# Kernel tuning notes

Hardware: AMD Instinct MI355X
Metric: run time of the kernel (lower is better)

## Reference

```python
import jax, jax.numpy as jnp
import numpy as np

V, E, HD, B, T, K = 50000, 256, 512, 64, 512, 16
H = HD // 2            # per-direction LSTM hidden size
START_IDX, STOP_IDX = K - 2, K - 1
NEG = -10000.0


def setup_inputs() -> dict:
    key = jax.random.key(0)
    ks = jax.random.split(key, 12)
    s = 0.05
    sentence = jax.random.randint(ks[0], (B, T), 0, V)
    emb = jax.random.normal(ks[1], (V, E), jnp.float32)
    w_ih_f = jax.random.normal(ks[2], (4 * H, E), jnp.float32) * s
    w_hh_f = jax.random.normal(ks[3], (4 * H, H), jnp.float32) * s
    b_f = jax.random.normal(ks[4], (4 * H,), jnp.float32) * s
    w_ih_b = jax.random.normal(ks[5], (4 * H, E), jnp.float32) * s
    w_hh_b = jax.random.normal(ks[6], (4 * H, H), jnp.float32) * s
    b_b = jax.random.normal(ks[7], (4 * H,), jnp.float32) * s
    w_out = jax.random.normal(ks[8], (K, HD), jnp.float32) * s
    b_out = jax.random.normal(ks[9], (K,), jnp.float32) * s
    transitions = jax.random.normal(ks[10], (K, K), jnp.float32)
    transitions = transitions.at[START_IDX, :].set(NEG)  # nothing transitions into START
    transitions = transitions.at[:, STOP_IDX].set(NEG)   # nothing transitions out of STOP
    return dict(sentence=sentence, emb=emb, w_ih_f=w_ih_f, w_hh_f=w_hh_f, b_f=b_f,
                w_ih_b=w_ih_b, w_hh_b=w_hh_b, b_b=b_b, w_out=w_out, b_out=b_out,
                transitions=transitions)


def _lstm(xs, w_ih, w_hh, b):
    # xs: [T, B, E] -> hs: [T, B, H]; PyTorch gate order i,f,g,o; bias b = b_ih + b_hh
    Bn = xs.shape[1]
    def step(carry, x):
        h, c = carry
        g = x @ w_ih.T + h @ w_hh.T + b
        i, f, gg, o = jnp.split(g, 4, axis=-1)
        c = jax.nn.sigmoid(f) * c + jax.nn.sigmoid(i) * jnp.tanh(gg)
        h = jax.nn.sigmoid(o) * jnp.tanh(c)
        return (h, c), h
    init = (jnp.zeros((Bn, H), xs.dtype), jnp.zeros((Bn, H), xs.dtype))
    return jax.lax.scan(step, init, xs)[1]


def _lstm_feats(sentence, emb, w_ih_f, w_hh_f, b_f, w_ih_b, w_hh_b, b_b, w_out, b_out):
    x = emb[sentence].transpose(1, 0, 2)                 # [T, B, E]
    hf = _lstm(x, w_ih_f, w_hh_f, b_f)                   # forward direction
    hb = _lstm(x[::-1], w_ih_b, w_hh_b, b_b)[::-1]       # backward direction
    h = jnp.concatenate([hf, hb], axis=-1)               # [T, B, HD]
    return h @ w_out.T + b_out                           # [T, B, K]


def _viterbi(feats, transitions):
    # feats: [T, B, K]
    Bn = feats.shape[1]
    init = jnp.full((Bn, K), NEG, jnp.float32).at[:, START_IDX].set(0.0)
    def vstep(fv, feat):
        scores = fv[:, None, :] + transitions[None, :, :]  # [B, next, prev]
        return jnp.max(scores, axis=2) + feat, jnp.argmax(scores, axis=2)
    fv, bptrs = jax.lax.scan(vstep, init, feats)           # bptrs: [T, B, K]
    terminal = fv + transitions[STOP_IDX][None, :]
    best_score = jnp.max(terminal, axis=1)                 # [B]
    best_tag = jnp.argmax(terminal, axis=1)                # [B]
    def bstep(tag, bptr):
        prev = jnp.take_along_axis(bptr, tag[:, None], axis=1)[:, 0]
        return prev, tag
    _, path = jax.lax.scan(bstep, best_tag, bptrs, reverse=True)  # [T, B]
    return best_score, path


def reference(sentence, emb, w_ih_f, w_hh_f, b_f, w_ih_b, w_hh_b, b_b, w_out, b_out, transitions):
    feats = _lstm_feats(sentence, emb, w_ih_f, w_hh_f, b_f, w_ih_b, w_hh_b, b_b, w_out, b_out)
    score, tag_seq = _viterbi(feats, transitions)
    return score, tag_seq
```

## Files before the change

kernel.cpp:

```cpp
#include <hip/hip_runtime.h>
#include <math.h>

typedef _Float16 h2_t  __attribute__((ext_vector_type(2)));
typedef _Float16 h8_t  __attribute__((ext_vector_type(8)));
typedef _Float16 h16_t __attribute__((ext_vector_type(16)));
typedef _Float16 h32_t __attribute__((ext_vector_type(32)));
typedef float    f4_t  __attribute__((ext_vector_type(4)));

#define T_ 512
#define B_ 64
#define E_ 256
#define H_ 256
#define G_ 1024
#define K_ 16
#define NEG_ (-10000.0f)
#define START_ 14
#define STOP_ 15

#if defined(__has_builtin)
#if __has_builtin(__builtin_amdgcn_fdot2)
#define HAVE_FDOT2 1
#endif
#endif

static __device__ __forceinline__ float dot2(h2_t a, h2_t b, float c) {
#ifdef HAVE_FDOT2
    return __builtin_amdgcn_fdot2(a, b, c, false);
#else
    return fmaf((float)a[0], (float)b[0], fmaf((float)a[1], (float)b[1], c));
#endif
}

template <int P, typename V>
static __device__ __forceinline__ h2_t get2(V v) {
    return __builtin_shufflevector(v, v, 2 * P, 2 * P + 1);
}

__global__ __launch_bounds__(256)
void prep_weights(const float* __restrict__ w_hh_f,
                  const float* __restrict__ w_hh_b,
                  const float* __restrict__ w_ih_f,
                  const float* __restrict__ w_ih_b,
                  _Float16* __restrict__ wreg,
                  _Float16* __restrict__ wlds,
                  _Float16* __restrict__ wih16)
{
    const int blk = blockIdx.x, tid = threadIdx.x;
    if (blk < 48) {
        int idx = blk * 256 + tid;
        int dir = idx / 6144, rem = idx % 6144;
        int v = rem / 512, q = rem % 512;
        int row = (v < 6) ? q : q + 512;
        int kb = (v % 6) * 32;
        const float* src = (dir ? w_hh_b : w_hh_f) + (size_t)row * 256 + kb;
        _Float16* dst = wreg + (size_t)idx * 32;
        #pragma unroll
        for (int i = 0; i < 32; ++i) dst[i] = (_Float16)src[i];
    } else if (blk < 112) {
        int idx = (blk - 48) * 256 + tid;
        int dir = idx / 8192, rem = idx % 8192;
        int j = rem / 512, q = rem % 512;
        int p = j / 8, c = j % 8;
        int row = (c < 4) ? q : q + 512;
        int kb = 192 + (c & 3) * 16 + p * 8;
        const float* src = (dir ? w_hh_b : w_hh_f) + (size_t)row * 256 + kb;
        _Float16* dst = wlds + (size_t)idx * 8;
        #pragma unroll
        for (int i = 0; i < 8; ++i) dst[i] = (_Float16)src[i];
    } else {
        int idx = (blk - 112) * 256 + tid;
        int dir = idx / 32768, rem = idx % 32768;
        const float* src = (dir ? w_ih_b : w_ih_f) + (size_t)rem * 8;
        _Float16* dst = wih16 + (size_t)idx * 8;
        #pragma unroll
        for (int i = 0; i < 8; ++i) dst[i] = (_Float16)src[i];
    }
}

__global__ __launch_bounds__(256)
void gates_mfma(const int* __restrict__ sentence,
                const float* __restrict__ emb,
                const _Float16* __restrict__ wih16,
                _Float16* __restrict__ gin_f,
                _Float16* __restrict__ gin_b)
{
    __shared__ _Float16 As[64 * 264];
    __shared__ _Float16 Bs[256 * 40];
    __shared__ int sidx[64];

    const int bm  = blockIdx.x;
    const int dir = blockIdx.y;
    const int tid = threadIdx.x;

    const _Float16* __restrict__ wih = wih16 + (size_t)dir * 262144;
    _Float16* __restrict__ gout      = dir ? gin_b : gin_f;

    if (tid < 64) sidx[tid] = sentence[tid * T_ + bm];
    __syncthreads();

    {
        const int r = tid & 63, kq = tid >> 6;
        const float4* src = (const float4*)(emb + (size_t)sidx[r] * 256 + kq * 64);
        _Float16* dst = As + r * 264 + kq * 64;
        #pragma unroll
        for (int c = 0; c < 8; ++c) {
            float4 v0 = src[2 * c], v1 = src[2 * c + 1];
            h8_t o;
            o[0] = (_Float16)v0.x; o[1] = (_Float16)v0.y;
            o[2] = (_Float16)v0.z; o[3] = (_Float16)v0.w;
            o[4] = (_Float16)v1.x; o[5] = (_Float16)v1.y;
            o[6] = (_Float16)v1.z; o[7] = (_Float16)v1.w;
            *(h8_t*)(dst + c * 8) = o;
        }
    }

    const int wave = tid >> 6, lane = tid & 63;
    const int l15 = lane & 15, quad = lane >> 4;

    for (int pass = 0; pass < 4; ++pass) {
        const int n0 = pass * 256;
        f4_t acc[16];
        #pragma unroll
        for (int nt = 0; nt < 16; ++nt) acc[nt] = (f4_t){0.f, 0.f, 0.f, 0.f};

        for (int kc = 0; kc < 8; ++kc) {
            __syncthreads();
            {
                const h8_t* bsrc = (const h8_t*)(wih + (size_t)(n0 + tid) * 256 + kc * 32);
                #pragma unroll
                for (int c = 0; c < 4; ++c)
                    *(h8_t*)(Bs + tid * 40 + c * 8) = bsrc[c];
            }
            __syncthreads();
            h8_t a = *(const h8_t*)(As + (wave * 16 + l15) * 264 + kc * 32 + quad * 8);
            #pragma unroll
            for (int nt = 0; nt < 16; ++nt) {
                h8_t b = *(const h8_t*)(Bs + (nt * 16 + l15) * 40 + quad * 8);
                acc[nt] = __builtin_amdgcn_mfma_f32_16x16x32_f16(a, b, acc[nt], 0, 0, 0);
            }
        }

        const size_t mbase = (size_t)bm * 64 + wave * 16 + quad * 4;
        #pragma unroll
        for (int nt = 0; nt < 16; ++nt) {
            const int col = n0 + nt * 16 + l15;
            #pragma unroll
            for (int r = 0; r < 4; ++r)
                gout[(mbase + r) * 1024 + col] = (_Float16)acc[nt][r];
        }
    }
}

#define D4R(W, X, HV, P0) do {                                                \
    h2_t p0 = get2<0>(HV), p1 = get2<1>(HV), p2 = get2<2>(HV), p3 = get2<3>(HV); \
    a0 = dot2(get2<(P0)+0>(W), p0, a0); a1 = dot2(get2<(P0)+0>(X), p0, a1);   \
    a0 = dot2(get2<(P0)+1>(W), p1, a0); a1 = dot2(get2<(P0)+1>(X), p1, a1);   \
    a0 = dot2(get2<(P0)+2>(W), p2, a0); a1 = dot2(get2<(P0)+2>(X), p2, a1);   \
    a0 = dot2(get2<(P0)+3>(W), p3, a0); a1 = dot2(get2<(P0)+3>(X), p3, a1);   \
} while (0)

#define GRP(W, X, BB) do {                                                    \
    h8_t v0 = HB[(BB) + 0], v1 = HB[(BB) + 1], v2 = HB[(BB) + 2], v3 = HB[(BB) + 3]; \
    D4R(W, X, v0, 0); D4R(W, X, v1, 4); D4R(W, X, v2, 8); D4R(W, X, v3, 12);  \
} while (0)

#define DLDS(C) do {                                                          \
    h8_t wA0 = WS8[((C)) * 512 + q];                                          \
    h8_t wB0 = WS8[((C) + 4) * 512 + q];                                      \
    h8_t wA1 = WS8[(8 + (C)) * 512 + q];                                      \
    h8_t wB1 = WS8[(8 + (C) + 4) * 512 + q];                                  \
    h8_t u0 = HB[24 + 2 * (C)], u1 = HB[24 + 2 * (C) + 1];                    \
    D4R(wA0, wB0, u0, 0); D4R(wA1, wB1, u1, 0);                               \
} while (0)

__global__ __launch_bounds__(512, 2)
void lstm_persist(const _Float16* __restrict__ gin_f,
                  const _Float16* __restrict__ gin_b,
                  const _Float16* __restrict__ wreg,
                  const _Float16* __restrict__ wlds,
                  const float* __restrict__ b_f,
                  const float* __restrict__ b_b,
                  float* __restrict__ hf, float* __restrict__ hb)
{
    __shared__ h8_t  wsh8[8192];
    __shared__ h8_t  hbuf8[32];
    __shared__ float gbuf[1024];

    const int dir = blockIdx.x >> 6;
    const int b   = blockIdx.x & 63;
    const int q   = threadIdx.x;

    const _Float16* __restrict__ gin = dir ? gin_b : gin_f;
    const float*    __restrict__ bs  = dir ? b_b : b_f;
    float*          __restrict__ hout = dir ? hb : hf;

    {
        const h8_t* src = (const h8_t*)wlds + (size_t)dir * 8192 + q;
        #pragma unroll
        for (int j = 0; j < 16; ++j) wsh8[j * 512 + q] = src[(size_t)j * 512];
    }

    const h32_t* wr = (const h32_t*)wreg + (size_t)dir * 6144 + q;
    h32_t W0 = wr[0 * 512], W1 = wr[1 * 512], W2 = wr[2 * 512];
    h32_t W3 = wr[3 * 512], W4 = wr[4 * 512], W5 = wr[5 * 512];
    h32_t X0 = wr[6 * 512], X1 = wr[7 * 512], X2 = wr[8 * 512];
    h32_t X3 = wr[9 * 512], X4 = wr[10 * 512], X5 = wr[11 * 512];

    const float bias0 = bs[q];
    const float bias1 = bs[q + 512];

    if (q < 32) {
        h8_t z = (h8_t)(_Float16)0.f;
        hbuf8[q] = z;
    }
    float c = 0.f;
    __syncthreads();

    const long tstr = 64 * 1024;
    const long hstr = 64 * 256;
    const _Float16* gp = gin + (size_t)(dir ? 511 : 0) * tstr + (size_t)b * 1024 + q;
    float*          hp = hout + (size_t)(dir ? 511 : 0) * hstr + (size_t)b * 256 + q;
    const long gstep = dir ? -tstr : tstr;
    const long hstep = dir ? -hstr : hstr;

    const h8_t* HB  = hbuf8;
    const h8_t* WS8 = wsh8;

    _Float16 gc0 = gp[0], gc1 = gp[512];

    for (int s = 0; s < T_; ++s) {
        _Float16 gn0 = gp[gstep], gn1 = gp[gstep + 512];

        float a0 = bias0 + (float)gc0;
        float a1 = bias1 + (float)gc1;

        GRP(W0, X0, 0);  GRP(W1, X1, 4);  GRP(W2, X2, 8);
        GRP(W3, X3, 12); GRP(W4, X4, 16); GRP(W5, X5, 20);
        DLDS(0); DLDS(1); DLDS(2); DLDS(3);

        gbuf[q] = a0;
        gbuf[q + 512] = a1;
        __syncthreads();
        if (q < 256) {
            float gi = gbuf[q], gf = gbuf[q + 256], gg = gbuf[q + 512], go = gbuf[q + 768];
            float si = 1.f / (1.f + expf(-gi));
            float sf = 1.f / (1.f + expf(-gf));
            float so = 1.f / (1.f + expf(-go));
            c = sf * c + si * tanhf(gg);
            float h = so * tanhf(c);
            hp[0] = h;
            ((_Float16*)hbuf8)[q] = (_Float16)h;
        }
        gc0 = gn0; gc1 = gn1;
        gp += gstep;
        hp += hstep;
        __syncthreads();
    }
}

__global__ __launch_bounds__(256)
void feats_proj(const float* __restrict__ hf, const float* __restrict__ hb,
                const float* __restrict__ w_out, const float* __restrict__ b_out,
                float* __restrict__ feats)
{
    const int lane = threadIdx.x & 63;
    const int wv   = threadIdx.x >> 6;
    const int m    = blockIdx.x * 4 + wv;
    const int o    = lane & 15;
    const int qq   = lane >> 4;

    const float* hsrc = (qq < 2) ? (hf + (size_t)m * 256 + qq * 128)
                                 : (hb + (size_t)m * 256 + (qq - 2) * 128);
    const float4* h4 = (const float4*)hsrc;
    const float4* w4 = (const float4*)(w_out + o * 512 + qq * 128);

    float acc = 0.f;
    #pragma unroll
    for (int i = 0; i < 32; ++i) {
        float4 hv = h4[i], wvv = w4[i];
        acc = fmaf(hv.x, wvv.x, acc);
        acc = fmaf(hv.y, wvv.y, acc);
        acc = fmaf(hv.z, wvv.z, acc);
        acc = fmaf(hv.w, wvv.w, acc);
    }
    acc += __shfl_xor(acc, 16, 64);
    acc += __shfl_xor(acc, 32, 64);
    if (lane < 16) feats[(size_t)m * 16 + o] = acc + b_out[o];
}

__global__ __launch_bounds__(64)
void viterbi(const float* __restrict__ feats, const float* __restrict__ trans,
             float* __restrict__ out)
{
    __shared__ unsigned char bp[T_][16];
    const int b    = blockIdx.x;
    const int lane = threadIdx.x;
    const int l15  = lane & 15;

    float tr[16];
    #pragma unroll
    for (int p = 0; p < 16; ++p)
        tr[p] = (lane < 16) ? trans[lane * 16 + p] : 0.f;

    float fv = (lane == START_) ? 0.f : NEG_;

    for (int t4 = 0; t4 < T_; t4 += 4) {
        float fblk = feats[((size_t)(t4 + (lane >> 4)) * 64 + b) * 16 + l15];
        #pragma unroll
        for (int tt = 0; tt < 4; ++tt) {
            const int t = t4 + tt;
            float best = -3.4e38f; int arg = 0;
            #pragma unroll
            for (int p = 0; p < 16; ++p) {
                float s = __shfl(fv, p, 64) + tr[p];
                if (s > best) { best = s; arg = p; }
            }
            float ft = __shfl(fblk, tt * 16 + l15, 64);
            if (lane < 16) {
                fv = best + ft;
                bp[t][lane] = (unsigned char)arg;
            }
        }
    }

    float term = fv + ((lane < 16) ? trans[STOP_ * 16 + lane] : 0.f);
    float v  = (lane < 16) ? term : -3.4e38f;
    int  idx = (lane < 16) ? lane : (1 << 20);
    #pragma unroll
    for (int off = 1; off < 64; off <<= 1) {
        float v2 = __shfl_xor(v, off, 64);
        int   i2 = __shfl_xor(idx, off, 64);
        if (v2 > v || (v2 == v && i2 < idx)) { v = v2; idx = i2; }
    }
    __syncthreads();
    if (lane == 0) {
        out[b] = v;
        int tag = idx;
        for (int t = T_ - 1; t >= 0; --t) {
            out[64 + (size_t)t * 64 + b] = (float)tag;
            tag = bp[t][tag];
        }
    }
}

extern "C" void kernel_launch(void* const* d_in, const int* in_sizes, int n_in,
                              void* d_out, int out_size, void* d_ws, size_t ws_size,
                              hipStream_t stream) {
    const int*   sentence = (const int*)d_in[0];
    const float* emb      = (const float*)d_in[1];
    const float* w_ih_f   = (const float*)d_in[2];
    const float* w_hh_f   = (const float*)d_in[3];
    const float* b_f      = (const float*)d_in[4];
    const float* w_ih_b   = (const float*)d_in[5];
    const float* w_hh_b   = (const float*)d_in[6];
    const float* b_b      = (const float*)d_in[7];
    const float* w_out    = (const float*)d_in[8];
    const float* b_out    = (const float*)d_in[9];
    const float* trans    = (const float*)d_in[10];
    float* out = (float*)d_out;

    _Float16* gin_f = (_Float16*)d_ws;
    _Float16* gin_b = gin_f + (size_t)T_ * B_ * G_;
    float* hf    = (float*)(gin_b + (size_t)T_ * B_ * G_);
    float* hb    = hf + (size_t)T_ * B_ * H_;
    float* feats = hb + (size_t)T_ * B_ * H_;
    _Float16* wreg  = (_Float16*)(feats + (size_t)T_ * B_ * K_);
    _Float16* wlds  = wreg + 393216;
    _Float16* wih16 = wlds + 131072;

    prep_weights<<<368, 256, 0, stream>>>(w_hh_f, w_hh_b, w_ih_f, w_ih_b,
                                          wreg, wlds, wih16);
    gates_mfma<<<dim3(512, 2), 256, 0, stream>>>(sentence, emb, wih16,
                                                 gin_f, gin_b);
    lstm_persist<<<128, 512, 0, stream>>>(gin_f, gin_b, wreg, wlds,
                                          b_f, b_b, hf, hb);
    feats_proj<<<8192, 256, 0, stream>>>(hf, hb, w_out, b_out, feats);
    viterbi<<<64, 64, 0, stream>>>(feats, trans, out);
}
```

Before: 1.640 ms.

## Split each LSTM sequence across two blocks exchanging hidden state via global flags

The persistent LSTM previously ran one 512-thread block per (direction, batch) pair, holding the whole recurrent weight matrix in registers plus LDS. Now each pair is split over two blocks, each owning half the hidden units, so all of a block's weights fit in registers and the LDS weight reads go away. After every timestep the two halves exchange their fp16 hidden states through a global buffer, preset to 0xFF by a memset, using relaxed agent-scope atomic stores and spin-polling. This doubles the block count to 256 to use more CUs, but adds a cross-block global round-trip on every step of the serial recurrence, a 32 MB memset, and a risk of deadlock if the paired blocks are not co-resident.

```diff
diff --git a/kernel.cpp b/kernel.cpp
--- a/kernel.cpp
+++ b/kernel.cpp
@@ -3,7 +3,6 @@
 
 typedef _Float16 h2_t  __attribute__((ext_vector_type(2)));
 typedef _Float16 h8_t  __attribute__((ext_vector_type(8)));
-typedef _Float16 h16_t __attribute__((ext_vector_type(16)));
 typedef _Float16 h32_t __attribute__((ext_vector_type(32)));
 typedef float    f4_t  __attribute__((ext_vector_type(4)));
 
@@ -41,34 +40,23 @@
                   const float* __restrict__ w_hh_b,
                   const float* __restrict__ w_ih_f,
                   const float* __restrict__ w_ih_b,
-                  _Float16* __restrict__ wreg,
-                  _Float16* __restrict__ wlds,
+                  _Float16* __restrict__ wreg2,
                   _Float16* __restrict__ wih16)
 {
     const int blk = blockIdx.x, tid = threadIdx.x;
-    if (blk < 48) {
-        int idx = blk * 256 + tid;
-        int dir = idx / 6144, rem = idx % 6144;
-        int v = rem / 512, q = rem % 512;
-        int row = (v < 6) ? q : q + 512;
-        int kb = (v % 6) * 32;
-        const float* src = (dir ? w_hh_b : w_hh_f) + (size_t)row * 256 + kb;
-        _Float16* dst = wreg + (size_t)idx * 32;
+    if (blk < 64) {
+        int e = blk * 256 + tid;
+        int q = e & 511;
+        int g = e >> 9;
+        int d2 = g >> 3, v = g & 7;
+        int dir = d2 >> 1, half = d2 & 1;
+        int row = (q >> 7) * 256 + half * 128 + (q & 127);
+        const float* src = (dir ? w_hh_b : w_hh_f) + (size_t)row * 256 + v * 32;
+        _Float16* dst = wreg2 + (size_t)e * 32;
         #pragma unroll
         for (int i = 0; i < 32; ++i) dst[i] = (_Float16)src[i];
-    } else if (blk < 112) {
-        int idx = (blk - 48) * 256 + tid;
-        int dir = idx / 8192, rem = idx % 8192;
-        int j = rem / 512, q = rem % 512;
-        int p = j / 8, c = j % 8;
-        int row = (c < 4) ? q : q + 512;
-        int kb = 192 + (c & 3) * 16 + p * 8;
-        const float* src = (dir ? w_hh_b : w_hh_f) + (size_t)row * 256 + kb;
-        _Float16* dst = wlds + (size_t)idx * 8;
-        #pragma unroll
-        for (int i = 0; i < 8; ++i) dst[i] = (_Float16)src[i];
     } else {
-        int idx = (blk - 112) * 256 + tid;
+        int idx = (blk - 64) * 256 + tid;
         int dir = idx / 32768, rem = idx % 32768;
         const float* src = (dir ? w_ih_b : w_ih_f) + (size_t)rem * 8;
         _Float16* dst = wih16 + (size_t)idx * 8;
@@ -151,107 +139,119 @@
     }
 }
 
-#define D4R(W, X, HV, P0) do {                                                \
-    h2_t p0 = get2<0>(HV), p1 = get2<1>(HV), p2 = get2<2>(HV), p3 = get2<3>(HV); \
-    a0 = dot2(get2<(P0)+0>(W), p0, a0); a1 = dot2(get2<(P0)+0>(X), p0, a1);   \
-    a0 = dot2(get2<(P0)+1>(W), p1, a0); a1 = dot2(get2<(P0)+1>(X), p1, a1);   \
-    a0 = dot2(get2<(P0)+2>(W), p2, a0); a1 = dot2(get2<(P0)+2>(X), p2, a1);   \
-    a0 = dot2(get2<(P0)+3>(W), p3, a0); a1 = dot2(get2<(P0)+3>(X), p3, a1);   \
+#define DOT8(W, P0, HV, ACC) do {                                   \
+    ACC = dot2(get2<(P0)+0>(W), get2<0>(HV), ACC);                  \
+    ACC = dot2(get2<(P0)+1>(W), get2<1>(HV), ACC);                  \
+    ACC = dot2(get2<(P0)+2>(W), get2<2>(HV), ACC);                  \
+    ACC = dot2(get2<(P0)+3>(W), get2<3>(HV), ACC);                  \
 } while (0)
 
-#define GRP(W, X, BB) do {                                                    \
-    h8_t v0 = HB[(BB) + 0], v1 = HB[(BB) + 1], v2 = HB[(BB) + 2], v3 = HB[(BB) + 3]; \
-    D4R(W, X, v0, 0); D4R(W, X, v1, 4); D4R(W, X, v2, 8); D4R(W, X, v3, 12);  \
+#define VBLK(W, VI) do {                                            \
+    h8_t hv0 = HB[(VI)*4+0], hv1 = HB[(VI)*4+1];                    \
+    h8_t hv2 = HB[(VI)*4+2], hv3 = HB[(VI)*4+3];                    \
+    DOT8(W, 0,  hv0, a0); DOT8(W, 4,  hv1, a1);                     \
+    DOT8(W, 8,  hv2, a2); DOT8(W, 12, hv3, a3);                     \
 } while (0)
 
-#define DLDS(C) do {                                                          \
-    h8_t wA0 = WS8[((C)) * 512 + q];                                          \
-    h8_t wB0 = WS8[((C) + 4) * 512 + q];                                      \
-    h8_t wA1 = WS8[(8 + (C)) * 512 + q];                                      \
-    h8_t wB1 = WS8[(8 + (C) + 4) * 512 + q];                                  \
-    h8_t u0 = HB[24 + 2 * (C)], u1 = HB[24 + 2 * (C) + 1];                    \
-    D4R(wA0, wB0, u0, 0); D4R(wA1, wB1, u1, 0);                               \
-} while (0)
-
-__global__ __launch_bounds__(512, 2)
-void lstm_persist(const _Float16* __restrict__ gin_f,
-                  const _Float16* __restrict__ gin_b,
-                  const _Float16* __restrict__ wreg,
-                  const _Float16* __restrict__ wlds,
-                  const float* __restrict__ b_f,
-                  const float* __restrict__ b_b,
-                  float* __restrict__ hf, float* __restrict__ hb)
-{
-    __shared__ h8_t  wsh8[8192];
+__global__ __attribute__((amdgpu_flat_work_group_size(512, 512),
+                          amdgpu_waves_per_eu(2, 2)))
+void lstm_pair(const _Float16* __restrict__ gin_f,
+               const _Float16* __restrict__ gin_b,
+               const _Float16* __restrict__ wreg2,
+               const float* __restrict__ b_f,
+               const float* __restrict__ b_b,
+               float* __restrict__ hf, float* __restrict__ hb,
+               unsigned int* __restrict__ hex)
+{
     __shared__ h8_t  hbuf8[32];
-    __shared__ float gbuf[1024];
-
-    const int dir = blockIdx.x >> 6;
-    const int b   = blockIdx.x & 63;
-    const int q   = threadIdx.x;
-
-    const _Float16* __restrict__ gin = dir ? gin_b : gin_f;
-    const float*    __restrict__ bs  = dir ? b_b : b_f;
+    __shared__ float gbuf[512];
+
+    const int bid  = blockIdx.x;
+    const int c16  = bid >> 4;
+    const int w16  = bid & 15;
+    const int half = w16 >> 3;
+    const int pair = c16 * 8 + (w16 & 7);
+    const int dir  = pair >> 6;
+    const int b    = pair & 63;
+    const int q    = threadIdx.x;
+
+    const int gcl = q >> 7, off = q & 127;
+    const int row = gcl * 256 + half * 128 + off;
+
+    const _Float16* __restrict__ gin  = dir ? gin_b : gin_f;
+    const float*    __restrict__ bs   = dir ? b_b : b_f;
     float*          __restrict__ hout = dir ? hb : hf;
 
-    {
-        const h8_t* src = (const h8_t*)wlds + (size_t)dir * 8192 + q;
-        #pragma unroll
-        for (int j = 0; j < 16; ++j) wsh8[j * 512 + q] = src[(size_t)j * 512];
-    }
-
-    const h32_t* wr = (const h32_t*)wreg + (size_t)dir * 6144 + q;
-    h32_t W0 = wr[0 * 512], W1 = wr[1 * 512], W2 = wr[2 * 512];
-    h32_t W3 = wr[3 * 512], W4 = wr[4 * 512], W5 = wr[5 * 512];
-    h32_t X0 = wr[6 * 512], X1 = wr[7 * 512], X2 = wr[8 * 512];
-    h32_t X3 = wr[9 * 512], X4 = wr[10 * 512], X5 = wr[11 * 512];
-
-    const float bias0 = bs[q];
-    const float bias1 = bs[q + 512];
-
-    if (q < 32) {
-        h8_t z = (h8_t)(_Float16)0.f;
-        hbuf8[q] = z;
-    }
+    const h32_t* wr = (const h32_t*)wreg2 + (size_t)(dir * 2 + half) * 4096 + q;
+    h32_t W0 = wr[0 * 512], W1 = wr[1 * 512], W2 = wr[2 * 512], W3 = wr[3 * 512];
+    h32_t W4 = wr[4 * 512], W5 = wr[5 * 512], W6 = wr[6 * 512], W7 = wr[7 * 512];
+
+    const float bias = bs[row];
+
+    if (q < 32) hbuf8[q] = (h8_t)(_Float16)0.f;
     float c = 0.f;
     __syncthreads();
 
     const long tstr = 64 * 1024;
     const long hstr = 64 * 256;
-    const _Float16* gp = gin + (size_t)(dir ? 511 : 0) * tstr + (size_t)b * 1024 + q;
-    float*          hp = hout + (size_t)(dir ? 511 : 0) * hstr + (size_t)b * 256 + q;
+    const int  t0   = dir ? (T_ - 1) : 0;
+    const _Float16* gp = gin + (size_t)t0 * tstr + (size_t)b * 1024 + row;
+    float*          hp = hout + (size_t)t0 * hstr + (size_t)b * 256 + half * 128 + q;
     const long gstep = dir ? -tstr : tstr;
     const long hstep = dir ? -hstr : hstr;
 
-    const h8_t* HB  = hbuf8;
-    const h8_t* WS8 = wsh8;
-
-    _Float16 gc0 = gp[0], gc1 = gp[512];
+    unsigned int* hexPub = hex + (size_t)pair * 65536 + (size_t)half * 64 + (q >> 1);
+    const int pi = (q >= 128 && q < 192) ? (q - 128) : 0;
+    const unsigned int* hexPoll =
+        hex + (size_t)pair * 65536 + (size_t)(1 - half) * 64 + pi;
+    const int pdst = (1 - half) * 64 + pi;
+
+    const h8_t* HB = hbuf8;
+    unsigned int* hbufU = (unsigned int*)hbuf8;
+    _Float16*    hbufH = (_Float16*)hbuf8;
+
+    _Float16 gc0 = gp[0];
 
     for (int s = 0; s < T_; ++s) {
-        _Float16 gn0 = gp[gstep], gn1 = gp[gstep + 512];
-
-        float a0 = bias0 + (float)gc0;
-        float a1 = bias1 + (float)gc1;
-
-        GRP(W0, X0, 0);  GRP(W1, X1, 4);  GRP(W2, X2, 8);
-        GRP(W3, X3, 12); GRP(W4, X4, 16); GRP(W5, X5, 20);
-        DLDS(0); DLDS(1); DLDS(2); DLDS(3);
-
-        gbuf[q] = a0;
-        gbuf[q + 512] = a1;
+        _Float16 gn0 = gp[gstep];
+
+        float a0 = 0.f, a1 = 0.f, a2 = 0.f, a3 = 0.f;
+        VBLK(W0, 0); VBLK(W1, 1); VBLK(W2, 2); VBLK(W3, 3);
+        VBLK(W4, 4); VBLK(W5, 5); VBLK(W6, 6); VBLK(W7, 7);
+
+        gbuf[q] = bias + (float)gc0 + ((a0 + a1) + (a2 + a3));
         __syncthreads();
-        if (q < 256) {
-            float gi = gbuf[q], gf = gbuf[q + 256], gg = gbuf[q + 512], go = gbuf[q + 768];
+
+        if (q < 128) {
+            float gi = gbuf[q], gf = gbuf[128 + q];
+            float gg = gbuf[256 + q], go = gbuf[384 + q];
             float si = 1.f / (1.f + expf(-gi));
             float sf = 1.f / (1.f + expf(-gf));
             float so = 1.f / (1.f + expf(-go));
             c = sf * c + si * tanhf(gg);
             float h = so * tanhf(c);
             hp[0] = h;
-            ((_Float16*)hbuf8)[q] = (_Float16)h;
-        }
-        gc0 = gn0; gc1 = gn1;
+            hbufH[half * 128 + q] = (_Float16)h;
+            if (s < T_ - 1) {
+                float hn = __shfl_down(h, 1, 64);
+                if ((q & 1) == 0) {
+                    h2_t pk; pk[0] = (_Float16)h; pk[1] = (_Float16)hn;
+                    __hip_atomic_store(hexPub + s * 128,
+                                       __builtin_bit_cast(unsigned int, pk),
+                                       __ATOMIC_RELAXED, __HIP_MEMORY_SCOPE_AGENT);
+                }
+            }
+        } else if (q < 192 && s < T_ - 1) {
+            const unsigned int* src = hexPoll + s * 128;
+            unsigned int u;
+            int guard = 0;
+            do {
+                u = __hip_atomic_load(src, __ATOMIC_RELAXED,
+                                      __HIP_MEMORY_SCOPE_AGENT);
+            } while (u == 0xFFFFFFFFu && ++guard < (1 << 20));
+            hbufU[pdst] = u;
+        }
+        gc0 = gn0;
         gp += gstep;
         hp += hstep;
         __syncthreads();
@@ -364,16 +364,17 @@
     float* hf    = (float*)(gin_b + (size_t)T_ * B_ * G_);
     float* hb    = hf + (size_t)T_ * B_ * H_;
     float* feats = hb + (size_t)T_ * B_ * H_;
-    _Float16* wreg  = (_Float16*)(feats + (size_t)T_ * B_ * K_);
-    _Float16* wlds  = wreg + 393216;
-    _Float16* wih16 = wlds + 131072;
-
-    prep_weights<<<368, 256, 0, stream>>>(w_hh_f, w_hh_b, w_ih_f, w_ih_b,
-                                          wreg, wlds, wih16);
+    _Float16* wih16 = (_Float16*)(feats + (size_t)T_ * B_ * K_);
+    _Float16* wreg2 = wih16 + 524288;
+    unsigned int* hex = (unsigned int*)(wreg2 + 524288);
+
+    prep_weights<<<320, 256, 0, stream>>>(w_hh_f, w_hh_b, w_ih_f, w_ih_b,
+                                          wreg2, wih16);
     gates_mfma<<<dim3(512, 2), 256, 0, stream>>>(sentence, emb, wih16,
                                                  gin_f, gin_b);
-    lstm_persist<<<128, 512, 0, stream>>>(gin_f, gin_b, wreg, wlds,
-                                          b_f, b_b, hf, hb);
+    hipMemsetAsync(hex, 0xFF, (size_t)33554432, stream);
+    lstm_pair<<<256, 512, 0, stream>>>(gin_f, gin_b, wreg2, b_f, b_b,
+                                       hf, hb, hex);
     feats_proj<<<8192, 256, 0, stream>>>(hf, hb, w_out, b_out, feats);
     viterbi<<<64, 64, 0, stream>>>(feats, trans, out);
 }
```

Result: faster. 1.371 ms (-16.4%).
